# Performance work log

Measured on AMD Instinct MI355X. Metric: run time of the kernel, lower is better.

Reference implementation:

```python
import jax, jax.numpy as jnp
import numpy as np

B, T, D = 4, 1024, 768
HW = 32            # H = W = sqrt(T)
DS = D // 16       # d_state = 48
CHUNK = 8          # items_each_chunk (must divide W)


def _ln(x, w, b, eps=1e-5):
    mu = x.mean(-1, keepdims=True)
    var = ((x - mu) ** 2).mean(-1, keepdims=True)
    return (x - mu) / jnp.sqrt(var + eps) * w + b


def _conv1x1(x, w):  # x: (B,C,H,W), w: (O,C)
    return jnp.einsum('bchw,oc->bohw', x, w)


def _dwconv(x, w, b, pad):  # depthwise conv, w: (C,1,k,k)
    y = jax.lax.conv_general_dilated(
        x, w, (1, 1), [(pad, pad), (pad, pad)],
        dimension_numbers=('NCHW', 'OIHW', 'NCHW'),
        feature_group_count=x.shape[1])
    if b is not None:
        y = y + b[None, :, None, None]
    return y


def _norm_gates(Gl, Gm, Gr):
    gl, gm, gr = jax.nn.sigmoid(Gl), jax.nn.sigmoid(Gm), jax.nn.sigmoid(Gr)
    s = gl + gm + gr
    s = s.at[:, :, 0, :].set(gm[:, :, 0, :] + gr[:, :, 0, :])    # top row: no h-1 neighbor
    s = s.at[:, :, -1, :].set(gl[:, :, -1, :] + gm[:, :, -1, :])  # bottom row: no h+1 neighbor
    s = jnp.maximum(s, 1e-7)
    return gl / s, gm / s, gr / s


def _gspn_scan(X, L, Gl, Gm, Gr, chunk):
    # GateRecurrent2dnoind: scan along W in independent chunks of `chunk` columns.
    # H[:, :, h, t] = L*X + Gl*Hprev[h-1] + Gm*Hprev[h] + Gr*Hprev[h+1], Hprev=0 at chunk start.
    b, c, h, w = X.shape
    nc = w // chunk

    def to_scan(a):  # (B,C,H,W) -> (chunk, B, C, H, nc)
        return a.reshape(b, c, h, nc, chunk).transpose(4, 0, 1, 2, 3)

    xs, ls, gls, gms, grs = map(to_scan, (X, L, Gl, Gm, Gr))

    def step(hprev, inp):
        x, l, gl, gm, gr = inp
        h_up = jnp.pad(hprev[:, :, :-1], ((0, 0), (0, 0), (1, 0), (0, 0)))
        h_dn = jnp.pad(hprev[:, :, 1:], ((0, 0), (0, 0), (0, 1), (0, 0)))
        hn = l * x + gl * h_up + gm * hprev + gr * h_dn
        return hn, hn

    _, ys = jax.lax.scan(step, jnp.zeros((b, c, h, nc), X.dtype), (xs, ls, gls, gms, grs))
    return ys.transpose(1, 2, 3, 4, 0).reshape(b, c, h, w)


def setup_inputs() -> dict:
    key = jax.random.key(0)
    ks = jax.random.split(key, 16)
    s = 0.02
    return {
        'hidden_states': jax.random.normal(ks[0], (B, T, D), jnp.float32),
        'norm_w': jnp.ones((D,), jnp.float32),
        'norm_b': jnp.zeros((D,), jnp.float32),
        'in_proj_w': jax.random.normal(ks[1], (D, D), jnp.float32) * s,
        'conv7_w': jax.random.normal(ks[2], (D, 1, 7, 7), jnp.float32) * s,
        'conv7_b': jnp.zeros((D,), jnp.float32),
        'xdown_w': jax.random.normal(ks[3], (DS, D), jnp.float32) * s,
        'wup_w': jax.random.normal(ks[4], (12 * D, DS), jnp.float32) * s,
        'lup_w': jax.random.normal(ks[5], (4 * D, DS), jnp.float32) * s,
        'uup_w': jax.random.normal(ks[6], (4 * D, DS), jnp.float32) * s,
        'dcoef_w': jax.random.normal(ks[7], (4 * D, DS), jnp.float32) * s,
        'm_w': jax.random.normal(ks[8], (4,), jnp.float32) * 0.25,
        'outconv_w': jax.random.normal(ks[9], (D, D), jnp.float32) * s,
        'outdconv_w': jax.random.normal(ks[10], (D, 1, 3, 3), jnp.float32) * s,
        'outproj_w': jax.random.normal(ks[11], (D, D), jnp.float32) * s,
    }


def reference(hidden_states, norm_w, norm_b, in_proj_w, conv7_w, conv7_b,
              xdown_w, wup_w, lup_w, uup_w, dcoef_w, m_w,
              outconv_w, outdconv_w, outproj_w):
    b, t, d = hidden_states.shape
    hh = ww = HW
    shortcut = hidden_states
    x = _ln(shortcut, norm_w, norm_b)                      # (B,T,D)
    x = x.transpose(0, 2, 1).reshape(b, d, hh, ww)         # (B,D,H,W)
    x = _conv1x1(x, in_proj_w)
    x = _dwconv(x, conv7_w, conv7_b, 3)
    xp = _conv1x1(x, xdown_w)                              # (B,ds,H,W)
    ws = _conv1x1(xp, wup_w)                               # (B,12D,H,W)
    Ls = _conv1x1(xp, lup_w)                               # (B,4D,H,W)
    Us = _conv1x1(xp, uup_w)
    Ds = _conv1x1(xp, dcoef_w)
    # 4 scan directions: [x, x^T, flip_w(x), flip_w(x^T)]
    x_hwwh = jnp.stack([x, x.transpose(0, 1, 3, 2)], axis=1)       # (B,2,D,H,W)
    xs = jnp.concatenate([x_hwwh, x_hwwh[..., ::-1]], axis=1)      # (B,4,D,H,W)
    xs = xs.reshape(b, 4 * d, hh, ww)
    Gl, Gm, Gr = ws[:, :4 * d], ws[:, 4 * d:8 * d], ws[:, 8 * d:]
    gl, gm, gr = _norm_gates(Gl, Gm, Gr)
    out = _gspn_scan(xs, Ls, gl, gm, gr, CHUNK)
    out = out * Us + xs * Ds
    out = out.reshape(b, 4, d, hh, ww)
    out = jnp.einsum('bkdhw,k->bdhw', out, m_w)            # m_conv (1x1 over 4 dirs)
    out = _conv1x1(out, outconv_w)
    out = _dwconv(out, outdconv_w, None, 1)
    out = out * jax.nn.relu(out)
    out = out.reshape(b, d, t).transpose(0, 2, 1)
    out = out @ outproj_w.T
    return out, shortcut
```

## Files before the change

kernel.cpp:

```cpp
#include <hip/hip_runtime.h>

typedef unsigned short u16;
typedef unsigned int u32;
typedef __attribute__((ext_vector_type(8))) short short8v;
typedef __attribute__((ext_vector_type(4))) float f32x4;

#define DD 768
#define PP 1024
#define NTOK 4096
#define ASN 520

__device__ __forceinline__ u16 f2bf(float f) {
  u32 u = __builtin_bit_cast(u32, f);
  u += 0x7fffu + ((u >> 16) & 1u);
  return (u16)(u >> 16);
}
__device__ __forceinline__ float b2f(u16 v) {
  return __builtin_bit_cast(float, (u32)v << 16);
}
__device__ __forceinline__ u32 pk_trunc(float fa, float fb) {
  return __builtin_amdgcn_perm(__builtin_bit_cast(u32, fa), __builtin_bit_cast(u32, fb), 0x07060302u);
}
__device__ __forceinline__ float ex8(const short8v& v, int j) {
  const u32 dw = ((const u32*)&v)[j >> 1];
  return __builtin_bit_cast(float, (j & 1) ? (dw & 0xffff0000u) : (dw << 16));
}

__global__ __launch_bounds__(256) void prep_ln_k(const float* __restrict__ hs,
                                                 const float* __restrict__ gw, const float* __restrict__ gb,
                                                 u16* __restrict__ lnout, float* __restrict__ shortcut,
                                                 const float* __restrict__ win, u16* __restrict__ wInB,
                                                 const float* __restrict__ wout, u16* __restrict__ wOutB,
                                                 const float* __restrict__ wprj, u16* __restrict__ wPrjB,
                                                 const float* __restrict__ xdw, u16* __restrict__ wXdB,
                                                 const float* __restrict__ wup, const float* __restrict__ lup,
                                                 const float* __restrict__ uup, const float* __restrict__ dco,
                                                 u16* __restrict__ wB) {
  const int id = blockIdx.x;
  const int t = threadIdx.x;
  if (id < 4096) {
    const int tok = id;
    const float* xr = hs + (size_t)tok * DD;
    float v0 = xr[t], v1 = xr[t + 256], v2 = xr[t + 512];
    float s = v0 + v1 + v2;
    float q = v0 * v0 + v1 * v1 + v2 * v2;
#pragma unroll
    for (int off = 32; off > 0; off >>= 1) {
      s += __shfl_down(s, off, 64);
      q += __shfl_down(q, off, 64);
    }
    __shared__ float ss[4], qs[4];
    const int wid = t >> 6, lane = t & 63;
    if (lane == 0) { ss[wid] = s; qs[wid] = q; }
    __syncthreads();
    const float st = ss[0] + ss[1] + ss[2] + ss[3];
    const float qt = qs[0] + qs[1] + qs[2] + qs[3];
    const float mu = st * (1.f / 768.f);
    const float var = qt * (1.f / 768.f) - mu * mu;
    const float rstd = rsqrtf(var + 1e-5f);
    float* sc = shortcut + (size_t)tok * DD;
    u16* lo = lnout + (size_t)tok * DD;
    sc[t] = v0; sc[t + 256] = v1; sc[t + 512] = v2;
    lo[t]       = f2bf((v0 - mu) * rstd * gw[t] + gb[t]);
    lo[t + 256] = f2bf((v1 - mu) * rstd * gw[t + 256] + gb[t + 256]);
    lo[t + 512] = f2bf((v2 - mu) * rstd * gw[t + 512] + gb[t + 512]);
    return;
  }
  const int id2 = id - 4096;
  if (id2 < 6912) {
    const int m = id2 / 2304;
    const int i = (id2 - m * 2304) * 256 + t;
    const float* s = (m == 0) ? win : (m == 1) ? wout : wprj;
    u16* d = (m == 0) ? wInB : (m == 1) ? wOutB : wPrjB;
    d[i] = f2bf(s[i]);
  } else if (id2 < 7104) {
    const int i = (id2 - 6912) * 256 + t;
    const int r = i / DD;
    wXdB[i] = (r < 48) ? f2bf(xdw[i]) : (u16)0;
  } else {
    const int c = id2 - 7104;
    u16* dst = wB + (size_t)c * 2048;
    for (int i = t; i < 2048; i += 256) {
      const int row = i >> 6, s = i & 63;
      u16 v = 0;
      if (row < 24 && s < 48) {
        const int k = row & 3, type = row >> 2;
        const int ch = k * DD + c;
        const float* src;
        if (type < 3) src = wup + ((size_t)(type * 3072 + ch)) * 48;
        else if (type == 3) src = lup + (size_t)ch * 48;
        else if (type == 4) src = uup + (size_t)ch * 48;
        else src = dco + (size_t)ch * 48;
        v = f2bf(src[s]);
      }
      dst[i] = v;
    }
  }
}

__global__ __launch_bounds__(256) void gemm_bf16(const u16* __restrict__ A,
                                                 const u16* __restrict__ Bt,
                                                 void* __restrict__ outv, const int mode) {
  __shared__ u16 Al[64][40];
  __shared__ u16 Bl[128][40];
  const int t = threadIdx.x;
  const int ntile = blockIdx.x * 128;
  const int mtile = blockIdx.y * 64;
  const int wid = t >> 6, lane = t & 63;
  const int m0 = (wid & 1) * 32, n0 = (wid >> 1) * 64;
  const int l15 = lane & 15, quad = lane >> 4;
  f32x4 acc[2][4];
#pragma unroll
  for (int mi = 0; mi < 2; ++mi)
#pragma unroll
    for (int ni = 0; ni < 4; ++ni) acc[mi][ni] = (f32x4){0.f, 0.f, 0.f, 0.f};
  const int ra = t >> 2, sa = t & 3;
  const int rb = t >> 1, hb = t & 1;
  const u16* ag = A + (size_t)(mtile + ra) * DD + sa * 8;
  const u16* bg = Bt + (size_t)(ntile + rb) * DD + hb * 16;
  for (int k0 = 0; k0 < DD; k0 += 32) {
    const uint4 av = *reinterpret_cast<const uint4*>(ag + k0);
    const uint4 bv0 = *reinterpret_cast<const uint4*>(bg + k0);
    const uint4 bv1 = *reinterpret_cast<const uint4*>(bg + k0 + 8);
    __syncthreads();
    *reinterpret_cast<uint4*>(&Al[ra][sa * 8]) = av;
    *reinterpret_cast<uint4*>(&Bl[rb][hb * 16]) = bv0;
    *reinterpret_cast<uint4*>(&Bl[rb][hb * 16 + 8]) = bv1;
    __syncthreads();
    short8v af[2];
#pragma unroll
    for (int mi = 0; mi < 2; ++mi)
      af[mi] = *reinterpret_cast<const short8v*>(&Al[m0 + mi * 16 + l15][quad * 8]);
    short8v bfr[4];
#pragma unroll
    for (int ni = 0; ni < 4; ++ni)
      bfr[ni] = *reinterpret_cast<const short8v*>(&Bl[n0 + ni * 16 + l15][quad * 8]);
#pragma unroll
    for (int mi = 0; mi < 2; ++mi)
#pragma unroll
      for (int ni = 0; ni < 4; ++ni)
        acc[mi][ni] = __builtin_amdgcn_mfma_f32_16x16x32_bf16(af[mi], bfr[ni], acc[mi][ni], 0, 0, 0);
  }
#pragma unroll
  for (int mi = 0; mi < 2; ++mi) {
#pragma unroll
    for (int ni = 0; ni < 4; ++ni) {
      const int ob = mtile + m0 + mi * 16 + quad * 4;
      const int pg = ntile + n0 + ni * 16 + l15;
      if (mode == 1) {
        *reinterpret_cast<f32x4*>((float*)outv + (size_t)pg * DD + ob) = acc[mi][ni];
      } else if (mode == 2) {
        const int bb = pg >> 10, pq = pg & 1023;
        const int q = ((pq & 31) >> 4) * 512 + (pq >> 5) * 16 + (pq & 15);
        u16* dst = (u16*)outv + ((size_t)(bb * 1024 + q)) * 64 + ob;
        const u32 lo = (u32)f2bf(acc[mi][ni][0]) | ((u32)f2bf(acc[mi][ni][1]) << 16);
        const u32 hi = (u32)f2bf(acc[mi][ni][2]) | ((u32)f2bf(acc[mi][ni][3]) << 16);
        *reinterpret_cast<uint2*>(dst) = make_uint2(lo, hi);
      } else {
        const int bb = pg >> 10, pq = pg & 1023;
        u16* dstb = (u16*)outv;
#pragma unroll
        for (int r = 0; r < 4; ++r)
          dstb[((size_t)(bb * DD + ob + r)) * PP + pq] = f2bf(acc[mi][ni][r]);
      }
    }
  }
}

__global__ __launch_bounds__(256) void dwconv7_k(const u16* __restrict__ x,
                                                 const float* __restrict__ wgt,
                                                 const float* __restrict__ bias,
                                                 u16* __restrict__ y) {
  const int bc = blockIdx.x;
  const int c = bc % DD;
  __shared__ float tile[38 * 38];
  __shared__ float wl[49];
  __shared__ float bsh[1];
  const int t = threadIdx.x;
  for (int i = t; i < 38 * 38; i += 256) tile[i] = 0.f;
  __syncthreads();
  const u16* xr = x + (size_t)bc * PP;
  for (int i = t; i < 512; i += 256) {
    const u32 v = reinterpret_cast<const u32*>(xr)[i];
    const int p0 = i * 2;
    const int h = p0 >> 5, w = p0 & 31;
    tile[(h + 3) * 38 + w + 3] = b2f((u16)v);
    tile[(h + 3) * 38 + w + 4] = b2f((u16)(v >> 16));
  }
  if (t < 49) wl[t] = wgt[c * 49 + t];
  if (t == 0) bsh[0] = bias[c];
  __syncthreads();
  u16* yo = y + (size_t)bc * PP;
  for (int i = t; i < 1024; i += 256) {
    const int h = i >> 5, w = i & 31;
    float acc = bsh[0];
#pragma unroll
    for (int kh = 0; kh < 7; ++kh)
#pragma unroll
      for (int kw = 0; kw < 7; ++kw)
        acc = fmaf(wl[kh * 7 + kw], tile[(h + kh) * 38 + (w + kw)], acc);
    yo[i] = f2bf(acc);
  }
}

__global__ __launch_bounds__(256) void dwconv3_k(const u16* __restrict__ x,
                                                 const float* __restrict__ wgt,
                                                 u16* __restrict__ y) {
  const int bc = blockIdx.x;
  const int c = bc % DD;
  __shared__ float tile[34 * 34];
  __shared__ float wl[9];
  const int t = threadIdx.x;
  for (int i = t; i < 34 * 34; i += 256) tile[i] = 0.f;
  __syncthreads();
  const u16* xr = x + (size_t)bc * PP;
  for (int i = t; i < 512; i += 256) {
    const u32 v = reinterpret_cast<const u32*>(xr)[i];
    const int p0 = i * 2;
    const int h = p0 >> 5, w = p0 & 31;
    tile[(h + 1) * 34 + w + 1] = b2f((u16)v);
    tile[(h + 1) * 34 + w + 2] = b2f((u16)(v >> 16));
  }
  if (t < 9) wl[t] = wgt[c * 9 + t];
  __syncthreads();
  u16* yo = y + (size_t)bc * PP;
  for (int i = t; i < 1024; i += 256) {
    const int h = i >> 5, w = i & 31;
    float acc = 0.f;
#pragma unroll
    for (int kh = 0; kh < 3; ++kh)
#pragma unroll
      for (int kw = 0; kw < 3; ++kw)
        acc = fmaf(wl[kh * 3 + kw], tile[(h + kh) * 34 + (w + kw)], acc);
    const float r = acc > 0.f ? acc * acc : 0.f;
    yo[i] = f2bf(r);
  }
}

__global__ __launch_bounds__(256, 5) void scan_k(const u16* __restrict__ y2b,
                                                 const u16* __restrict__ xpA,
                                                 const u16* __restrict__ wB,
                                                 const float* __restrict__ mwp,
                                                 u16* __restrict__ out1) {
  const int bid = blockIdx.x;
  const int bc = bid >> 1;
  const int half = bid & 1;
  const int b = bc / DD;
  const int c = bc - b * DD;
  __shared__ u16 act[24 * ASN];
  __shared__ u16 planeb[32][34];
  __shared__ u16 planeTb[32][34];
  __shared__ u16 outpb[2][16][34];
  const int t = threadIdx.x;
  const int wid = t >> 6, lane = t & 63, l15 = lane & 15, quad = lane >> 4;
  {
    const u16* yp = y2b + (size_t)bc * PP;
    for (int i = t; i < 512; i += 256) {
      const u32 v = reinterpret_cast<const u32*>(yp)[i];
      const int p0 = i * 2;
      const int hh = p0 >> 5, ww = p0 & 31;
      *reinterpret_cast<u32*>(&planeb[hh][ww]) = v;
      planeTb[ww][hh] = (u16)v;
      planeTb[ww + 1][hh] = (u16)(v >> 16);
    }
  }
  {
    const u16* wc = wB + (size_t)c * 2048;
    short8v bw[2][2];
#pragma unroll
    for (int nt = 0; nt < 2; ++nt)
#pragma unroll
      for (int ks = 0; ks < 2; ++ks)
        bw[nt][ks] = *reinterpret_cast<const short8v*>(wc + (nt * 16 + l15) * 64 + ks * 32 + quad * 8);
    const u16* ab = xpA + ((size_t)(b * 1024 + half * 512 + wid * 128)) * 64;
#pragma unroll 4
    for (int mt = 0; mt < 8; ++mt) {
      const u16* ar = ab + (mt * 16 + l15) * 64 + quad * 8;
      const short8v a0 = *reinterpret_cast<const short8v*>(ar);
      const short8v a1 = *reinterpret_cast<const short8v*>(ar + 32);
      f32x4 acc0 = {0.f, 0.f, 0.f, 0.f}, acc1 = {0.f, 0.f, 0.f, 0.f};
      acc0 = __builtin_amdgcn_mfma_f32_16x16x32_bf16(a0, bw[0][0], acc0, 0, 0, 0);
      acc0 = __builtin_amdgcn_mfma_f32_16x16x32_bf16(a1, bw[0][1], acc0, 0, 0, 0);
      acc1 = __builtin_amdgcn_mfma_f32_16x16x32_bf16(a0, bw[1][0], acc1, 0, 0, 0);
      acc1 = __builtin_amdgcn_mfma_f32_16x16x32_bf16(a1, bw[1][1], acc1, 0, 0, 0);
      const int qb = wid * 128 + mt * 16 + quad * 4;
      *reinterpret_cast<uint2*>(&act[l15 * ASN + qb]) =
          make_uint2(pk_trunc(acc0[1], acc0[0]), pk_trunc(acc0[3], acc0[2]));
      if (l15 < 8)
        *reinterpret_cast<uint2*>(&act[(16 + l15) * ASN + qb]) =
            make_uint2(pk_trunc(acc1[1], acc1[0]), pk_trunc(acc1[3], acc1[2]));
    }
  }
  __syncthreads();
  const int dpair = wid & 1;
  const int ncl = wid >> 1;
  const int d = lane >> 5;
  const int h = lane & 31;
  const int k = dpair * 2 + d;
  const float mw = mwp[k];
  const int base16 = h * 16 + ncl * 8;
  const short8v vGl = *reinterpret_cast<const short8v*>(&act[(0  + k) * ASN + base16]);
  const short8v vGm = *reinterpret_cast<const short8v*>(&act[(4  + k) * ASN + base16]);
  const short8v vGr = *reinterpret_cast<const short8v*>(&act[(8  + k) * ASN + base16]);
  const short8v vL  = *reinterpret_cast<const short8v*>(&act[(12 + k) * ASN + base16]);
  const short8v vU  = *reinterpret_cast<const short8v*>(&act[(16 + k) * ASN + base16]);
  const short8v vD  = *reinterpret_cast<const short8v*>(&act[(20 + k) * ASN + base16]);
  const u16* prow = (d == 0) ? &planeb[h][0] : &planeTb[h][0];
  const bool top = (h == 0), bot = (h == 31);
  float gl[8], gm[8], gr[8], Lx[8], xvv[8];
#pragma unroll
  for (int j = 0; j < 8; ++j) {
    const int w = half * 16 + ncl * 8 + j;
    const int wc_ = dpair ? (31 - w) : w;
    const float xv = b2f(prow[wc_]);
    float el = __expf(-ex8(vGl, j));
    const float em = __expf(-ex8(vGm, j));
    float er = __expf(-ex8(vGr, j));
    if (top) el = 1e30f;
    if (bot) er = 1e30f;
    const float pl = 1.f + el, pm = 1.f + em, pr = 1.f + er;
    const float ul = pm * pr, um = pl * pr, ur = pl * pm;
    const float rcpS = __builtin_amdgcn_rcpf(ul + um + ur);
    gl[j] = ul * rcpS; gm[j] = um * rcpS; gr[j] = ur * rcpS;
    Lx[j] = ex8(vL, j) * xv;
    xvv[j] = xv;
  }
  float H = 0.f;
#pragma unroll
  for (int j = 0; j < 8; ++j) {
    const float up = __shfl(H, lane - 1, 64);
    const float dn = __shfl(H, lane + 1, 64);
    H = fmaf(gl[j], up, fmaf(gm[j], H, fmaf(gr[j], dn, Lx[j])));
    float part = fmaf(H, ex8(vU, j), xvv[j] * ex8(vD, j)) * mw;
    part += __shfl_xor(part, 32, 64);
    if (d == 0)
      outpb[dpair][ncl * 8 + j][h] = (u16)(__builtin_bit_cast(u32, part) >> 16);
  }
  __syncthreads();
  const int hh = t >> 3, wp = t & 7;
  const float v0 = b2f(outpb[0][wp * 2][hh]) + b2f(outpb[1][wp * 2][hh]);
  const float v1 = b2f(outpb[0][wp * 2 + 1][hh]) + b2f(outpb[1][wp * 2 + 1][hh]);
  const u32 pk = pk_trunc(v1, v0);
  *reinterpret_cast<u32*>(out1 + (size_t)bc * PP + hh * 32 + half * 16 + wp * 2) = pk;
}

__global__ __launch_bounds__(256) void transpose_bf16(const u16* __restrict__ in,
                                                      u16* __restrict__ out) {
  __shared__ u16 tile[64][72];
  const int b = blockIdx.z;
  const int c0 = blockIdx.y * 64;
  const int p0 = blockIdx.x * 64;
  const int t = threadIdx.x;
  const int r = t >> 2, s2 = t & 3;
  const u16* src = in + ((size_t)(b * DD + c0 + r)) * PP + p0 + s2 * 16;
  *reinterpret_cast<uint4*>(&tile[r][s2 * 16]) = *reinterpret_cast<const uint4*>(src);
  *reinterpret_cast<uint4*>(&tile[r][s2 * 16 + 8]) = *reinterpret_cast<const uint4*>(src + 8);
  __syncthreads();
  const int pr = t >> 2, cs = t & 3;
  union { u16 u[16]; uint4 v[2]; } vals;
#pragma unroll
  for (int i = 0; i < 16; ++i) vals.u[i] = tile[cs * 16 + i][pr];
  u16* dst = out + ((size_t)(b * 1024 + p0 + pr)) * DD + c0 + cs * 16;
  reinterpret_cast<uint4*>(dst)[0] = vals.v[0];
  reinterpret_cast<uint4*>(dst)[1] = vals.v[1];
}

extern "C" void kernel_launch(void* const* d_in, const int* in_sizes, int n_in,
                              void* d_out, int out_size, void* d_ws, size_t ws_size,
                              hipStream_t stream) {
  const float* hs   = (const float*)d_in[0];
  const float* nw   = (const float*)d_in[1];
  const float* nb   = (const float*)d_in[2];
  const float* win  = (const float*)d_in[3];
  const float* c7w  = (const float*)d_in[4];
  const float* c7b  = (const float*)d_in[5];
  const float* xdw  = (const float*)d_in[6];
  const float* wupw = (const float*)d_in[7];
  const float* lupw = (const float*)d_in[8];
  const float* uupw = (const float*)d_in[9];
  const float* dcow = (const float*)d_in[10];
  const float* mww  = (const float*)d_in[11];
  const float* wout = (const float*)d_in[12];
  const float* odw  = (const float*)d_in[13];
  const float* wprj = (const float*)d_in[14];
  float* out0 = (float*)d_out;
  float* shortcut = out0 + (size_t)NTOK * DD;

  char* ws = (char*)d_ws;
  u16* lnA    = (u16*)(ws + 0);
  u16* wInB   = (u16*)(ws + 6291456);
  u16* wOutB  = (u16*)(ws + 7471104);
  u16* wPrjB  = (u16*)(ws + 8650752);
  u16* wB     = (u16*)(ws + 9830400);
  u16* wXdB   = (u16*)(ws + 12976128);
  u16* xpA    = (u16*)(ws + 13074432);
  u16* y1b    = (u16*)(ws + 13598720);
  u16* y2b    = (u16*)(ws + 19890176);
  u16* y2t    = (u16*)(ws + 26181632);
  u16* out1   = (u16*)(ws + 32473088);
  u16* out1T  = lnA;
  u16* y3b    = y1b;
  u16* y4b    = y2b;
  u16* y4T    = y2t;

  prep_ln_k<<<11968, 256, 0, stream>>>(hs, nw, nb, lnA, shortcut,
                                       win, wInB, wout, wOutB, wprj, wPrjB,
                                       xdw, wXdB, wupw, lupw, uupw, dcow, wB);
  gemm_bf16<<<dim3(32, 12), 256, 0, stream>>>(wInB, lnA, y1b, 3);
  dwconv7_k<<<3072, 256, 0, stream>>>(y1b, c7w, c7b, y2b);
  transpose_bf16<<<dim3(16, 12, 4), 256, 0, stream>>>(y2b, y2t);
  gemm_bf16<<<dim3(32, 1), 256, 0, stream>>>(wXdB, y2t, xpA, 2);
  scan_k<<<6144, 256, 0, stream>>>(y2b, xpA, wB, mww, out1);
  transpose_bf16<<<dim3(16, 12, 4), 256, 0, stream>>>(out1, out1T);
  gemm_bf16<<<dim3(32, 12), 256, 0, stream>>>(wOutB, out1T, y3b, 3);
  dwconv3_k<<<3072, 256, 0, stream>>>(y3b, odw, y4b);
  transpose_bf16<<<dim3(16, 12, 4), 256, 0, stream>>>(y4b, y4T);
  gemm_bf16<<<dim3(32, 12), 256, 0, stream>>>(wPrjB, y4T, out0, 1);
}
```

Measured before the change: 263.0 us.

## Fuse transposes into GEMM B-loads and add dedicated xdown GEMM kernel

Removes the three standalone transpose kernels. The GEMMs now read channel-major activations directly and transpose them into padded shared memory while staging. A new small-tile xdgemm_k replaces the one-row-block GEMM for the 48-channel projection so that more blocks run in parallel. The scan kernel loads each row as one vector read, and the neighbour shuffles become DPP row shifts. The cost is scattered 32-bit LDS writes and strided global B loads inside the GEMM loop.

```diff
diff --git a/kernel.cpp b/kernel.cpp
--- a/kernel.cpp
+++ b/kernel.cpp
@@ -98,14 +98,16 @@
   }
 }
 
+template <int BSRC>
 __global__ __launch_bounds__(256) void gemm_bf16(const u16* __restrict__ A,
                                                  const u16* __restrict__ Bt,
                                                  void* __restrict__ outv, const int mode) {
   __shared__ u16 Al[64][40];
-  __shared__ u16 Bl[128][40];
+  __shared__ u16 BlF[144 * 40];
   const int t = threadIdx.x;
   const int ntile = blockIdx.x * 128;
   const int mtile = blockIdx.y * 64;
+  const int bb = ntile >> 10, pq0 = ntile & 1023;
   const int wid = t >> 6, lane = t & 63;
   const int m0 = (wid & 1) * 32, n0 = (wid >> 1) * 64;
   const int l15 = lane & 15, quad = lane >> 4;
@@ -115,17 +117,37 @@
 #pragma unroll
     for (int ni = 0; ni < 4; ++ni) acc[mi][ni] = (f32x4){0.f, 0.f, 0.f, 0.f};
   const int ra = t >> 2, sa = t & 3;
+  const u16* ag = A + (size_t)(mtile + ra) * DD + sa * 8;
   const int rb = t >> 1, hb = t & 1;
-  const u16* ag = A + (size_t)(mtile + ra) * DD + sa * 8;
   const u16* bg = Bt + (size_t)(ntile + rb) * DD + hb * 16;
+  const int chp = t >> 4, tokg = t & 15, tok0 = tokg * 8;
+  const u16* bgc = Bt + ((size_t)(bb * DD + chp * 2)) * PP + pq0 + tok0;
   for (int k0 = 0; k0 < DD; k0 += 32) {
     const uint4 av = *reinterpret_cast<const uint4*>(ag + k0);
-    const uint4 bv0 = *reinterpret_cast<const uint4*>(bg + k0);
-    const uint4 bv1 = *reinterpret_cast<const uint4*>(bg + k0 + 8);
+    uint4 bv0, bv1;
+    if (BSRC == 0) {
+      bv0 = *reinterpret_cast<const uint4*>(bg + k0);
+      bv1 = *reinterpret_cast<const uint4*>(bg + k0 + 8);
+    } else {
+      bv0 = *reinterpret_cast<const uint4*>(bgc + (size_t)k0 * PP);
+      bv1 = *reinterpret_cast<const uint4*>(bgc + (size_t)(k0 + 1) * PP);
+    }
     __syncthreads();
     *reinterpret_cast<uint4*>(&Al[ra][sa * 8]) = av;
-    *reinterpret_cast<uint4*>(&Bl[rb][hb * 16]) = bv0;
-    *reinterpret_cast<uint4*>(&Bl[rb][hb * 16 + 8]) = bv1;
+    if (BSRC == 0) {
+      const int pr = rb + (rb >> 3);
+      *reinterpret_cast<uint4*>(&BlF[pr * 40 + hb * 16]) = bv0;
+      *reinterpret_cast<uint4*>(&BlF[pr * 40 + hb * 16 + 8]) = bv1;
+    } else {
+      union { uint4 v; u16 u[8]; } ua, ub;
+      ua.v = bv0; ub.v = bv1;
+#pragma unroll
+      for (int i2 = 0; i2 < 8; ++i2) {
+        const int tk = tok0 + i2;
+        *reinterpret_cast<u32*>(&BlF[(tk + (tk >> 3)) * 40 + chp * 2]) =
+            (u32)ua.u[i2] | ((u32)ub.u[i2] << 16);
+      }
+    }
     __syncthreads();
     short8v af[2];
 #pragma unroll
@@ -133,8 +155,10 @@
       af[mi] = *reinterpret_cast<const short8v*>(&Al[m0 + mi * 16 + l15][quad * 8]);
     short8v bfr[4];
 #pragma unroll
-    for (int ni = 0; ni < 4; ++ni)
-      bfr[ni] = *reinterpret_cast<const short8v*>(&Bl[n0 + ni * 16 + l15][quad * 8]);
+    for (int ni = 0; ni < 4; ++ni) {
+      const int tl = n0 + ni * 16 + l15;
+      bfr[ni] = *reinterpret_cast<const short8v*>(&BlF[(tl + (tl >> 3)) * 40 + quad * 8]);
+    }
 #pragma unroll
     for (int mi = 0; mi < 2; ++mi)
 #pragma unroll
@@ -149,15 +173,8 @@
       const int pg = ntile + n0 + ni * 16 + l15;
       if (mode == 1) {
         *reinterpret_cast<f32x4*>((float*)outv + (size_t)pg * DD + ob) = acc[mi][ni];
-      } else if (mode == 2) {
-        const int bb = pg >> 10, pq = pg & 1023;
-        const int q = ((pq & 31) >> 4) * 512 + (pq >> 5) * 16 + (pq & 15);
-        u16* dst = (u16*)outv + ((size_t)(bb * 1024 + q)) * 64 + ob;
-        const u32 lo = (u32)f2bf(acc[mi][ni][0]) | ((u32)f2bf(acc[mi][ni][1]) << 16);
-        const u32 hi = (u32)f2bf(acc[mi][ni][2]) | ((u32)f2bf(acc[mi][ni][3]) << 16);
-        *reinterpret_cast<uint2*>(dst) = make_uint2(lo, hi);
       } else {
-        const int bb = pg >> 10, pq = pg & 1023;
+        const int pq = pg & 1023;
         u16* dstb = (u16*)outv;
 #pragma unroll
         for (int r = 0; r < 4; ++r)
@@ -165,6 +182,45 @@
       }
     }
   }
+}
+
+__global__ __launch_bounds__(256) void xdgemm_k(const u16* __restrict__ A,
+                                                const u16* __restrict__ Ycm,
+                                                u16* __restrict__ xpA) {
+  __shared__ u16 Al[64][72];
+  __shared__ u16 Bl[16][72];
+  const int t = threadIdx.x;
+  const int ntile = blockIdx.x * 16;
+  const int bb = ntile >> 10, pq0 = ntile & 1023;
+  const int wid = t >> 6, lane = t & 63, l15 = lane & 15, quad = lane >> 4;
+  f32x4 acc = (f32x4){0.f, 0.f, 0.f, 0.f};
+  const int arow = t >> 2, aks = (t & 3) * 16;
+  const u16* ag = A + (size_t)arow * DD + aks;
+  const int chp = t >> 3;
+  const int tk0 = (t & 7) * 2;
+  const u16* bg0 = Ycm + ((size_t)(bb * DD + chp * 2)) * PP + pq0 + tk0;
+  for (int k0 = 0; k0 < DD; k0 += 64) {
+    const uint4 a0 = *reinterpret_cast<const uint4*>(ag + k0);
+    const uint4 a1 = *reinterpret_cast<const uint4*>(ag + k0 + 8);
+    const u32 b0 = *reinterpret_cast<const u32*>(bg0 + (size_t)k0 * PP);
+    const u32 b1 = *reinterpret_cast<const u32*>(bg0 + (size_t)(k0 + 1) * PP);
+    __syncthreads();
+    *reinterpret_cast<uint4*>(&Al[arow][aks]) = a0;
+    *reinterpret_cast<uint4*>(&Al[arow][aks + 8]) = a1;
+    *reinterpret_cast<u32*>(&Bl[tk0][chp * 2]) = (b0 & 0xffffu) | (b1 << 16);
+    *reinterpret_cast<u32*>(&Bl[tk0 + 1][chp * 2]) = (b0 >> 16) | (b1 & 0xffff0000u);
+    __syncthreads();
+#pragma unroll
+    for (int ks = 0; ks < 2; ++ks) {
+      const short8v af = *reinterpret_cast<const short8v*>(&Al[wid * 16 + l15][ks * 32 + quad * 8]);
+      const short8v bf = *reinterpret_cast<const short8v*>(&Bl[l15][ks * 32 + quad * 8]);
+      acc = __builtin_amdgcn_mfma_f32_16x16x32_bf16(af, bf, acc, 0, 0, 0);
+    }
+  }
+  const int pq = pq0 + l15;
+  const int i = ((pq & 31) >> 4) * 512 + (pq >> 5) * 16 + (pq & 15);
+  u16* dst = xpA + ((size_t)(bb * 1024 + i)) * 64 + wid * 16 + quad * 4;
+  *reinterpret_cast<uint2*>(dst) = make_uint2(pk_trunc(acc[1], acc[0]), pk_trunc(acc[3], acc[2]));
 }
 
 __global__ __launch_bounds__(256) void dwconv7_k(const u16* __restrict__ x,
@@ -248,8 +304,8 @@
   const int b = bc / DD;
   const int c = bc - b * DD;
   __shared__ u16 act[24 * ASN];
-  __shared__ u16 planeb[32][34];
-  __shared__ u16 planeTb[32][34];
+  __shared__ u16 planeb[32][40];
+  __shared__ u16 planeTb[32][40];
   __shared__ u16 outpb[2][16][34];
   const int t = threadIdx.x;
   const int wid = t >> 6, lane = t & 63, l15 = lane & 15, quad = lane >> 4;
@@ -305,14 +361,14 @@
   const short8v vL  = *reinterpret_cast<const short8v*>(&act[(12 + k) * ASN + base16]);
   const short8v vU  = *reinterpret_cast<const short8v*>(&act[(16 + k) * ASN + base16]);
   const short8v vD  = *reinterpret_cast<const short8v*>(&act[(20 + k) * ASN + base16]);
-  const u16* prow = (d == 0) ? &planeb[h][0] : &planeTb[h][0];
+  const int wst = dpair ? (24 - half * 16 - ncl * 8) : (half * 16 + ncl * 8);
+  const u16* prowp = (d == 0) ? &planeb[h][wst] : &planeTb[h][wst];
+  const short8v vP = *reinterpret_cast<const short8v*>(prowp);
   const bool top = (h == 0), bot = (h == 31);
   float gl[8], gm[8], gr[8], Lx[8], xvv[8];
 #pragma unroll
   for (int j = 0; j < 8; ++j) {
-    const int w = half * 16 + ncl * 8 + j;
-    const int wc_ = dpair ? (31 - w) : w;
-    const float xv = b2f(prow[wc_]);
+    const float xv = ex8(vP, dpair ? (7 - j) : j);
     float el = __expf(-ex8(vGl, j));
     const float em = __expf(-ex8(vGm, j));
     float er = __expf(-ex8(vGr, j));
@@ -328,8 +384,11 @@
   float H = 0.f;
 #pragma unroll
   for (int j = 0; j < 8; ++j) {
-    const float up = __shfl(H, lane - 1, 64);
-    const float dn = __shfl(H, lane + 1, 64);
+    const int Hb = __builtin_bit_cast(int, H);
+    const float up = __builtin_bit_cast(float,
+        __builtin_amdgcn_update_dpp(0, Hb, 0x138, 0xf, 0xf, true));
+    const float dn = __builtin_bit_cast(float,
+        __builtin_amdgcn_update_dpp(0, Hb, 0x130, 0xf, 0xf, true));
     H = fmaf(gl[j], up, fmaf(gm[j], H, fmaf(gr[j], dn, Lx[j])));
     float part = fmaf(H, ex8(vU, j), xvv[j] * ex8(vD, j)) * mw;
     part += __shfl_xor(part, 32, 64);
@@ -342,27 +401,6 @@
   const float v1 = b2f(outpb[0][wp * 2 + 1][hh]) + b2f(outpb[1][wp * 2 + 1][hh]);
   const u32 pk = pk_trunc(v1, v0);
   *reinterpret_cast<u32*>(out1 + (size_t)bc * PP + hh * 32 + half * 16 + wp * 2) = pk;
-}
-
-__global__ __launch_bounds__(256) void transpose_bf16(const u16* __restrict__ in,
-                                                      u16* __restrict__ out) {
-  __shared__ u16 tile[64][72];
-  const int b = blockIdx.z;
-  const int c0 = blockIdx.y * 64;
-  const int p0 = blockIdx.x * 64;
-  const int t = threadIdx.x;
-  const int r = t >> 2, s2 = t & 3;
-  const u16* src = in + ((size_t)(b * DD + c0 + r)) * PP + p0 + s2 * 16;
-  *reinterpret_cast<uint4*>(&tile[r][s2 * 16]) = *reinterpret_cast<const uint4*>(src);
-  *reinterpret_cast<uint4*>(&tile[r][s2 * 16 + 8]) = *reinterpret_cast<const uint4*>(src + 8);
-  __syncthreads();
-  const int pr = t >> 2, cs = t & 3;
-  union { u16 u[16]; uint4 v[2]; } vals;
-#pragma unroll
-  for (int i = 0; i < 16; ++i) vals.u[i] = tile[cs * 16 + i][pr];
-  u16* dst = out + ((size_t)(b * 1024 + p0 + pr)) * DD + c0 + cs * 16;
-  reinterpret_cast<uint4*>(dst)[0] = vals.v[0];
-  reinterpret_cast<uint4*>(dst)[1] = vals.v[1];
 }
 
 extern "C" void kernel_launch(void* const* d_in, const int* in_sizes, int n_in,
@@ -396,24 +434,18 @@
   u16* xpA    = (u16*)(ws + 13074432);
   u16* y1b    = (u16*)(ws + 13598720);
   u16* y2b    = (u16*)(ws + 19890176);
-  u16* y2t    = (u16*)(ws + 26181632);
-  u16* out1   = (u16*)(ws + 32473088);
-  u16* out1T  = lnA;
+  u16* out1   = (u16*)(ws + 26181632);
   u16* y3b    = y1b;
-  u16* y4b    = y2b;
-  u16* y4T    = y2t;
+  u16* y4b    = out1;
 
   prep_ln_k<<<11968, 256, 0, stream>>>(hs, nw, nb, lnA, shortcut,
                                        win, wInB, wout, wOutB, wprj, wPrjB,
                                        xdw, wXdB, wupw, lupw, uupw, dcow, wB);
-  gemm_bf16<<<dim3(32, 12), 256, 0, stream>>>(wInB, lnA, y1b, 3);
+  gemm_bf16<0><<<dim3(32, 12), 256, 0, stream>>>(wInB, lnA, y1b, 3);
   dwconv7_k<<<3072, 256, 0, stream>>>(y1b, c7w, c7b, y2b);
-  transpose_bf16<<<dim3(16, 12, 4), 256, 0, stream>>>(y2b, y2t);
-  gemm_bf16<<<dim3(32, 1), 256, 0, stream>>>(wXdB, y2t, xpA, 2);
+  xdgemm_k<<<256, 256, 0, stream>>>(wXdB, y2b, xpA);
   scan_k<<<6144, 256, 0, stream>>>(y2b, xpA, wB, mww, out1);
-  transpose_bf16<<<dim3(16, 12, 4), 256, 0, stream>>>(out1, out1T);
-  gemm_bf16<<<dim3(32, 12), 256, 0, stream>>>(wOutB, out1T, y3b, 3);
+  gemm_bf16<1><<<dim3(32, 12), 256, 0, stream>>>(wOutB, out1, y3b, 3);
   dwconv3_k<<<3072, 256, 0, stream>>>(y3b, odw, y4b);
-  transpose_bf16<<<dim3(16, 12, 4), 256, 0, stream>>>(y4b, y4T);
-  gemm_bf16<<<dim3(32, 12), 256, 0, stream>>>(wPrjB, y4T, out0, 1);
-}
+  gemm_bf16<1><<<dim3(32, 12), 256, 0, stream>>>(wPrjB, y4b, out0, 1);
+}
```

Result: faster. 248.3 us (-5.6%).
